# Kernel optimization log

Hardware: AMD Instinct MI355X
Metric: run time of the kernel (lower is better)

Reference implementation:

```python
import jax, jax.numpy as jnp
import numpy as np
import math

B, T, M, C = 4, 2048, 16, 256   # batch, seq, m chunks, c_s chunk width
DIM = 1024                       # layer width; k = DIM // C = 4
D = 64                           # conditioning bottleneck
N_ITERS, TAU = 20, 1.0


def _diag_bias(rows, cols):
    b = np.full((rows, cols), -8.0, dtype=np.float32)
    for i in range(min(rows, cols)):
        b[i, i] = 0.0
    return jnp.asarray(b)


def setup_inputs() -> dict:
    key = jax.random.key(0)
    ks = jax.random.split(key, 10)
    state_dim = M * C
    k = DIM // C
    H_post = np.full((M, k), -8.0, dtype=np.float32)
    for i in range(M):
        H_post[i, i % k] = 0.0
    return {
        "s": jax.random.normal(ks[0], (B, T, M, C), jnp.float32),
        "gamma": 0.02 * jax.random.normal(ks[1], (state_dim,), jnp.float32),
        "compress": 0.02 * jax.random.normal(ks[2], (state_dim, D), jnp.float32),
        "alpha_pre": jnp.float32(0.01),
        "to_logits_pre": 0.02 * jax.random.normal(ks[3], (D, k * M), jnp.float32),
        "H_pre": _diag_bias(k, M),
        "alpha_align": jnp.float32(0.01),
        "to_logits_align": 0.02 * jax.random.normal(ks[4], (D, M * M), jnp.float32),
        "H_align": _diag_bias(M, M),
        "alpha_next": jnp.float32(0.01),
        "to_logits_next": 0.02 * jax.random.normal(ks[5], (D, M * M), jnp.float32),
        "H_next": _diag_bias(M, M),
        "alpha_post": jnp.float32(0.01),
        "to_logits_post": 0.02 * jax.random.normal(ks[6], (D, M * k), jnp.float32),
        "H_post": jnp.asarray(H_post),
        "W_layer": jax.random.normal(ks[7], (DIM, DIM), jnp.float32) / math.sqrt(DIM),
    }


def sinkhorn_log(logits, num_iters=N_ITERS, tau=TAU):
    """Log-domain Sinkhorn; output row-scaled so row sums = 1 * rows-normalized."""
    rows, cols = logits.shape[-2], logits.shape[-1]
    Z = logits / tau
    lr = -math.log(rows)
    lc = -math.log(cols)
    u0 = jnp.zeros(Z.shape[:-1], Z.dtype)
    v0 = jnp.zeros(Z.shape[:-2] + (cols,), Z.dtype)

    def body(_, uv):
        u, v = uv
        u = lr - jax.nn.logsumexp(Z + v[..., None, :], axis=-1)
        v = lc - jax.nn.logsumexp(Z + u[..., None], axis=-2)
        return (u, v)

    u, v = jax.lax.fori_loop(0, num_iters, body, (u0, v0))
    return jnp.exp(Z + u[..., None] + v[..., None, :]) * rows


def _route(code, alpha, to_logits, bias, state, rows, cols):
    """Fused: Sinkhorn(alpha*(code@to_logits)+bias) @ state."""
    raw = (code @ to_logits).reshape(code.shape[:-1] + (rows, cols))
    P = sinkhorn_log(alpha * raw + bias)
    return jnp.einsum('...ij,...jc->...ic', P, state)


def reference(s, gamma, compress, alpha_pre, to_logits_pre, H_pre,
              alpha_align, to_logits_align, H_align,
              alpha_next, to_logits_next, H_next,
              alpha_post, to_logits_post, H_post, W_layer):
    b, t, m, c = s.shape
    state_dim = m * c
    k = W_layer.shape[0] // c
    # RMSNorm over flattened state: F.normalize * sqrt(dim) * (gamma + 1)
    s_vec = s.reshape(b, t, state_dim)
    l2 = jnp.sqrt(jnp.sum(s_vec * s_vec, axis=-1, keepdims=True))
    s_norm = s_vec / jnp.maximum(l2, 1e-12) * jnp.sqrt(jnp.float32(state_dim)) * (gamma + 1.0)
    code = s_norm @ compress  # (b, t, d)
    # read: H_pre (k x m) routes state -> layer input
    layer_in = _route(code, alpha_pre, to_logits_pre, H_pre, s, k, m).reshape(b, t, k * c)
    layer_out = layer_in @ W_layer  # the wrapped layer_fn (dense linear)
    # write: align, absorb output via H_post, prepare next via H_next
    s_aligned = _route(code, alpha_align, to_logits_align, H_align, s, m, m)
    out_flat = layer_out.reshape(b, t, k, c)
    s_updated = s_aligned + _route(code, alpha_post, to_logits_post, H_post, out_flat, m, k)
    s_next = _route(code, alpha_next, to_logits_next, H_next, s_updated, m, m)
    return s_next
```

## Files before the change

kernel.cpp:

```cpp
#include <hip/hip_runtime.h>
#include <math.h>

#define NTOK 8192
#define SD   4096
#define ITERS 20

typedef __attribute__((ext_vector_type(8))) short short8;
typedef __attribute__((ext_vector_type(8))) unsigned short ushort8;
typedef __attribute__((ext_vector_type(4))) unsigned short us4;
typedef __attribute__((ext_vector_type(4))) float f32x4;

__device__ inline unsigned short f2bf(float x) {
    unsigned int u = __float_as_uint(x);
    unsigned int r = (u + 0x7FFFu + ((u >> 16) & 1u)) >> 16;
    return (unsigned short)r;
}
__device__ inline float bf2f(unsigned short u) {
    return __uint_as_float((unsigned int)u << 16);
}
__device__ inline void async_cp16(const void* gsrc, void* ldst) {
    __builtin_amdgcn_global_load_lds(
        (const __attribute__((address_space(1))) unsigned int*)gsrc,
        (__attribute__((address_space(3))) unsigned int*)ldst, 16, 0, 0);
}

__global__ __launch_bounds__(256) void k_preall(const float* __restrict__ W, unsigned short* __restrict__ WT,
                                                const float* __restrict__ compress, const float* __restrict__ gamma,
                                                unsigned short* __restrict__ cgT,
                                                const float* __restrict__ tl_pre, const float* __restrict__ tl_al,
                                                const float* __restrict__ tl_nx,  const float* __restrict__ tl_po,
                                                unsigned short* __restrict__ tlT)
{
    const int b = blockIdx.x;
    const int tid = threadIdx.x;
    if (b < 256) {
        __shared__ float tb[64][65];
        const int k0 = (b >> 4) * 64, n0 = (b & 15) * 64;
        #pragma unroll 4
        for (int q = 0; q < 16; ++q) {
            const int idx = q * 256 + tid;
            const int r = idx >> 6, c = idx & 63;
            tb[r][c] = W[(size_t)(k0 + r) * 1024 + n0 + c];
        }
        __syncthreads();
        #pragma unroll 4
        for (int q = 0; q < 16; ++q) {
            const int idx = q * 256 + tid;
            const int n = idx >> 6, k = idx & 63;
            WT[(size_t)(n0 + n) * 1024 + k0 + k] = f2bf(tb[k][n]);
        }
    } else if (b < 320) {
        __shared__ float tb2[64][65];
        __shared__ float gsh[64];
        const int k0 = (b - 256) * 64;
        #pragma unroll 4
        for (int q = 0; q < 16; ++q) {
            const int idx = q * 256 + tid;
            const int r = idx >> 6, dd = idx & 63;
            tb2[r][dd] = compress[(size_t)(k0 + r) * 64 + dd];
        }
        if (tid < 64) gsh[tid] = gamma[k0 + tid] + 1.0f;
        __syncthreads();
        #pragma unroll 4
        for (int q = 0; q < 16; ++q) {
            const int idx = q * 256 + tid;
            const int d = idx >> 6, r = idx & 63;
            cgT[(size_t)d * SD + k0 + r] = f2bf(tb2[r][d] * gsh[r]);
        }
    } else {
        const int idx = (b - 320) * 256 + tid;
        const int k = idx / 640, n = idx - k * 640;
        float v;
        if (n < 64)       v = tl_pre[k * 64 + n];
        else if (n < 320) v = tl_al[k * 256 + (n - 64)];
        else if (n < 576) v = tl_nx[k * 256 + (n - 320)];
        else              v = tl_po[k * 64 + (n - 576)];
        tlT[(size_t)n * 64 + k] = f2bf(v);
    }
}

__global__ __launch_bounds__(256) void k_code5(const float* __restrict__ s,
                                               const unsigned short* __restrict__ cgT,
                                               float* __restrict__ code_part,
                                               float* __restrict__ ssq_part)
{
    __shared__ float red[4 * 16 * 68];
    __shared__ float ssq_lds[64];
    const int tid  = threadIdx.x;
    const int lane = tid & 63;
    const int wid  = tid >> 6;
    const int q    = blockIdx.x;
    const int tok0 = blockIdx.y * 16;
    const int row  = lane & 15;
    const int kq   = lane >> 4;
    const int wk   = wid * 32;
    const int kbase = q * 1024;

    float ssq = 0.f;
    f32x4 acc[4];
    #pragma unroll
    for (int ni = 0; ni < 4; ++ni) acc[ni] = (f32x4){0.f, 0.f, 0.f, 0.f};

    const float*          srow  = s   + (size_t)(tok0 + row) * SD + kbase + wk + kq * 8;
    const unsigned short* cgrow = cgT + kbase + wk + kq * 8;

    #pragma unroll
    for (int ks = 0; ks < 8; ++ks) {
        const int kg = ks * 128;
        float4 v0 = *(const float4*)(srow + kg);
        float4 v1 = *(const float4*)(srow + kg + 4);
        ssq += v0.x*v0.x + v0.y*v0.y + v0.z*v0.z + v0.w*v0.w
             + v1.x*v1.x + v1.y*v1.y + v1.z*v1.z + v1.w*v1.w;
        short8 a;
        a[0]=(short)f2bf(v0.x); a[1]=(short)f2bf(v0.y); a[2]=(short)f2bf(v0.z); a[3]=(short)f2bf(v0.w);
        a[4]=(short)f2bf(v1.x); a[5]=(short)f2bf(v1.y); a[6]=(short)f2bf(v1.z); a[7]=(short)f2bf(v1.w);
        short8 b[4];
        #pragma unroll
        for (int ni = 0; ni < 4; ++ni)
            b[ni] = *(const short8*)(cgrow + (size_t)(ni * 16 + row) * SD + kg);
        #pragma unroll
        for (int ni = 0; ni < 4; ++ni)
            acc[ni] = __builtin_amdgcn_mfma_f32_16x16x32_bf16(a, b[ni], acc[ni], 0, 0, 0);
    }

    ssq += __shfl_xor(ssq, 16);
    ssq += __shfl_xor(ssq, 32);
    if (lane < 16) ssq_lds[wid * 16 + row] = ssq;

    #pragma unroll
    for (int ni = 0; ni < 4; ++ni)
        #pragma unroll
        for (int r = 0; r < 4; ++r)
            red[wid * 1088 + ((lane >> 4) * 4 + r) * 68 + ni * 16 + (lane & 15)] = acc[ni][r];
    __syncthreads();
    if (tid < 16)
        ssq_part[(size_t)q * NTOK + tok0 + tid] =
            ssq_lds[tid] + ssq_lds[16 + tid] + ssq_lds[32 + tid] + ssq_lds[48 + tid];
    #pragma unroll
    for (int q2 = 0; q2 < 4; ++q2) {
        const int idx = q2 * 256 + tid;
        const int tok = idx >> 6, d = idx & 63;
        float v = red[0 * 1088 + tok * 68 + d] + red[1 * 1088 + tok * 68 + d]
                + red[2 * 1088 + tok * 68 + d] + red[3 * 1088 + tok * 68 + d];
        code_part[((size_t)q * NTOK + tok0 + tok) * 64 + d] = v;
    }
}

#define LGS 660
__global__ __launch_bounds__(256) void k_sink5(const float* __restrict__ s,
                                               const float* __restrict__ code_part,
                                               const float* __restrict__ ssq_part,
                                               const unsigned short* __restrict__ tlT,
                                               const float* __restrict__ a_pre_p, const float* __restrict__ H_pre,
                                               const float* __restrict__ a_al_p,  const float* __restrict__ H_al,
                                               const float* __restrict__ a_nx_p,  const float* __restrict__ H_nx,
                                               const float* __restrict__ a_po_p,  const float* __restrict__ H_po,
                                               unsigned short* __restrict__ layer_in,
                                               float* __restrict__ Pna, float* __restrict__ Pnp)
{
    __shared__ __align__(16) char smem[48576];
    unsigned short* code_sh = (unsigned short*)(smem);
    unsigned short* lg_sh   = (unsigned short*)(smem + 2304);
    float*          Pnx_sh  = (float*)(smem + 2304);
    float*          Pal_sh  = (float*)(smem + 23424);
    float*          Ppo_sh  = (float*)(smem + 40064);
    float*          ssq_sh  = (float*)(smem + 44416);
    float*          Ppre_sh = (float*)(smem + 44480);

    const int tid  = threadIdx.x;
    const int lane = tid & 63;
    const int wid  = tid >> 6;
    const int tok0 = blockIdx.x * 16;

    float cv[4];
    #pragma unroll
    for (int q2 = 0; q2 < 4; ++q2) {
        const int idx = q2 * 256 + tid;
        const size_t off = (size_t)(tok0 + (idx >> 6)) * 64 + (idx & 63);
        cv[q2] = code_part[off] + code_part[(size_t)NTOK * 64 + off]
               + code_part[(size_t)2 * NTOK * 64 + off] + code_part[(size_t)3 * NTOK * 64 + off];
    }
    if (tid < 16) {
        float t = ssq_part[tok0 + tid] + ssq_part[NTOK + tok0 + tid]
                + ssq_part[2 * NTOK + tok0 + tid] + ssq_part[3 * NTOK + tok0 + tid];
        ssq_sh[tid] = 64.0f / fmaxf(sqrtf(t), 1e-12f);
    }
    __syncthreads();
    #pragma unroll
    for (int q2 = 0; q2 < 4; ++q2) {
        const int idx = q2 * 256 + tid;
        code_sh[(idx >> 6) * 72 + (idx & 63)] = f2bf(cv[q2] * ssq_sh[idx >> 6]);
    }
    __syncthreads();

    {
        f32x4 acc2[10];
        #pragma unroll
        for (int ni = 0; ni < 10; ++ni) acc2[ni] = (f32x4){0.f, 0.f, 0.f, 0.f};
        const int nbase = wid * 160;
        #pragma unroll
        for (int ks = 0; ks < 2; ++ks) {
            const int ko = ks * 32 + (lane >> 4) * 8;
            short8 a = *(const short8*)(code_sh + (lane & 15) * 72 + ko);
            #pragma unroll
            for (int ni = 0; ni < 10; ++ni) {
                short8 b = *(const short8*)(tlT + (size_t)(nbase + ni * 16 + (lane & 15)) * 64 + ko);
                acc2[ni] = __builtin_amdgcn_mfma_f32_16x16x32_bf16(a, b, acc2[ni], 0, 0, 0);
            }
        }
        #pragma unroll
        for (int ni = 0; ni < 10; ++ni)
            #pragma unroll
            for (int r = 0; r < 4; ++r)
                lg_sh[((lane >> 4) * 4 + r) * LGS + nbase + ni * 16 + (lane & 15)] = f2bf(acc2[ni][r]);
    }
    __syncthreads();

    const int t_in = lane >> 2;
    const int sub  = lane & 3;
    float Km[4][16];

    if (wid < 2) {
        const unsigned short* lgp = lg_sh + t_in * LGS + (wid == 0 ? 64 : 320) + sub * 64;
        #pragma unroll
        for (int rr = 0; rr < 4; ++rr)
            #pragma unroll
            for (int h = 0; h < 2; ++h) {
                ushort8 rv = *(const ushort8*)(lgp + rr * 16 + h * 8);
                #pragma unroll
                for (int e = 0; e < 8; ++e) Km[rr][h * 8 + e] = bf2f(rv[e]);
            }
    } else if (wid == 2) {
        const unsigned short* lgp = lg_sh + t_in * LGS + sub * 16;
        #pragma unroll
        for (int h = 0; h < 2; ++h) {
            ushort8 rv = *(const ushort8*)(lgp + h * 8);
            #pragma unroll
            for (int e = 0; e < 8; ++e) Km[0][h * 8 + e] = bf2f(rv[e]);
        }
    } else {
        const unsigned short* lgp = lg_sh + t_in * LGS + 576 + sub * 16;
        #pragma unroll
        for (int rr = 0; rr < 4; ++rr) {
            us4 rv = *(const us4*)(lgp + rr * 4);
            #pragma unroll
            for (int e = 0; e < 4; ++e) Km[rr][e] = bf2f(rv[e]);
        }
    }
    __syncthreads();

    if (wid < 2) {
        const float alpha = (wid == 0) ? (*a_al_p) : (*a_nx_p);
        const float* Hp   = ((wid == 0) ? H_al : H_nx) + sub * 64;
        #pragma unroll
        for (int rr = 0; rr < 4; ++rr)
            #pragma unroll
            for (int c = 0; c < 16; ++c)
                Km[rr][c] = __expf(alpha * Km[rr][c] + Hp[rr * 16 + c]);
        float v[16], u[4];
        #pragma unroll
        for (int c = 0; c < 16; ++c) v[c] = 1.0f;
        for (int it = 0; it < ITERS; ++it) {
            #pragma unroll
            for (int rr = 0; rr < 4; ++rr) {
                float su = 0.f;
                #pragma unroll
                for (int c = 0; c < 16; ++c) su += Km[rr][c] * v[c];
                u[rr] = 0.0625f * __builtin_amdgcn_rcpf(su);
            }
            float pv[16];
            #pragma unroll
            for (int c = 0; c < 16; ++c)
                pv[c] = Km[0][c]*u[0] + Km[1][c]*u[1] + Km[2][c]*u[2] + Km[3][c]*u[3];
            #pragma unroll
            for (int c = 0; c < 16; ++c) pv[c] += __shfl_xor(pv[c], 1);
            #pragma unroll
            for (int c = 0; c < 16; ++c) pv[c] += __shfl_xor(pv[c], 2);
            #pragma unroll
            for (int c = 0; c < 16; ++c) v[c] = 0.0625f * __builtin_amdgcn_rcpf(pv[c]);
        }
        float* dst = ((wid == 0) ? Pal_sh : Pnx_sh) + t_in * 260;
        #pragma unroll
        for (int rr = 0; rr < 4; ++rr) {
            const float su16 = 16.0f * u[rr];
            #pragma unroll
            for (int c = 0; c < 16; ++c)
                dst[(sub * 4 + rr) * 16 + c] = Km[rr][c] * su16 * v[c];
        }
    } else if (wid == 2) {
        const float alpha = *a_pre_p;
        const float* Hp  = H_pre + sub * 16;
        #pragma unroll
        for (int c = 0; c < 16; ++c) Km[0][c] = __expf(alpha * Km[0][c] + Hp[c]);
        float v[16], u;
        #pragma unroll
        for (int c = 0; c < 16; ++c) v[c] = 1.0f;
        for (int it = 0; it < ITERS; ++it) {
            float su = 0.f;
            #pragma unroll
            for (int c = 0; c < 16; ++c) su += Km[0][c] * v[c];
            u = 0.25f * __builtin_amdgcn_rcpf(su);
            float pv[16];
            #pragma unroll
            for (int c = 0; c < 16; ++c) pv[c] = Km[0][c] * u;
            #pragma unroll
            for (int c = 0; c < 16; ++c) pv[c] += __shfl_xor(pv[c], 1);
            #pragma unroll
            for (int c = 0; c < 16; ++c) pv[c] += __shfl_xor(pv[c], 2);
            #pragma unroll
            for (int c = 0; c < 16; ++c) v[c] = 0.0625f * __builtin_amdgcn_rcpf(pv[c]);
        }
        const float su4 = 4.0f * u;
        #pragma unroll
        for (int c = 0; c < 16; ++c)
            Ppre_sh[t_in * 64 + sub * 16 + c] = Km[0][c] * su4 * v[c];
    } else {
        const float alpha = *a_po_p;
        const float* Hp  = H_po + sub * 16;
        #pragma unroll
        for (int rr = 0; rr < 4; ++rr)
            #pragma unroll
            for (int c = 0; c < 4; ++c)
                Km[rr][c] = __expf(alpha * Km[rr][c] + Hp[rr * 4 + c]);
        float v[4], u[4];
        #pragma unroll
        for (int c = 0; c < 4; ++c) v[c] = 1.0f;
        for (int it = 0; it < ITERS; ++it) {
            #pragma unroll
            for (int rr = 0; rr < 4; ++rr) {
                float su = 0.f;
                #pragma unroll
                for (int c = 0; c < 4; ++c) su += Km[rr][c] * v[c];
                u[rr] = 0.0625f * __builtin_amdgcn_rcpf(su);
            }
            float pv[4];
            #pragma unroll
            for (int c = 0; c < 4; ++c)
                pv[c] = Km[0][c]*u[0] + Km[1][c]*u[1] + Km[2][c]*u[2] + Km[3][c]*u[3];
            #pragma unroll
            for (int c = 0; c < 4; ++c) pv[c] += __shfl_xor(pv[c], 1);
            #pragma unroll
            for (int c = 0; c < 4; ++c) pv[c] += __shfl_xor(pv[c], 2);
            #pragma unroll
            for (int c = 0; c < 4; ++c) v[c] = 0.25f * __builtin_amdgcn_rcpf(pv[c]);
        }
        #pragma unroll
        for (int rr = 0; rr < 4; ++rr) {
            const float su16 = 16.0f * u[rr];
            #pragma unroll
            for (int c = 0; c < 4; ++c)
                Ppo_sh[t_in * 68 + (sub * 4 + rr) * 4 + c] = Km[rr][c] * su16 * v[c];
        }
    }
    __syncthreads();

    const int ct = tid >> 4;
    const int cj = tid & 15;
    {
        const float* pnx = Pnx_sh + ct * 260;
        const float* pal = Pal_sh + ct * 260;
        const float* ppo = Ppo_sh + ct * 68;
        #pragma unroll
        for (int m = 0; m < 16; ++m) {
            float a2 = 0.f;
            #pragma unroll
            for (int t2 = 0; t2 < 16; ++t2) a2 += pnx[m * 16 + t2] * pal[t2 * 16 + cj];
            Pna[(size_t)(tok0 + ct) * 256 + m * 16 + cj] = a2;
        }
        #pragma unroll
        for (int e = 0; e < 4; ++e) {
            const int idx = cj * 4 + e;
            const int m = idx >> 2, q = idx & 3;
            float a2 = 0.f;
            #pragma unroll
            for (int t2 = 0; t2 < 16; ++t2) a2 += pnx[m * 16 + t2] * ppo[t2 * 4 + q];
            Pnp[(size_t)(tok0 + ct) * 64 + idx] = a2;
        }
    }

    #pragma unroll
    for (int g = 0; g < 4; ++g) {
        const int t = g * 4 + wid;
        const float4* sp = (const float4*)(s + (size_t)(tok0 + t) * SD) + lane;
        const float* pp = Ppre_sh + t * 64;
        f32x4 acc4[4];
        #pragma unroll
        for (int i = 0; i < 4; ++i) acc4[i] = (f32x4){0.f, 0.f, 0.f, 0.f};
        #pragma unroll
        for (int jh = 0; jh < 2; ++jh) {
            float4 sv[8];
            #pragma unroll
            for (int j = 0; j < 8; ++j) sv[j] = sp[(jh * 8 + j) * 64];
            #pragma unroll
            for (int i = 0; i < 4; ++i)
                #pragma unroll
                for (int j = 0; j < 8; ++j) {
                    const float pij = pp[i * 16 + jh * 8 + j];
                    acc4[i][0] += pij * sv[j].x;
                    acc4[i][1] += pij * sv[j].y;
                    acc4[i][2] += pij * sv[j].z;
                    acc4[i][3] += pij * sv[j].w;
                }
        }
        unsigned short* lo = layer_in + (size_t)(tok0 + t) * 1024 + lane * 4;
        #pragma unroll
        for (int i = 0; i < 4; ++i) {
            us4 o;
            o[0] = f2bf(acc4[i][0]); o[1] = f2bf(acc4[i][1]);
            o[2] = f2bf(acc4[i][2]); o[3] = f2bf(acc4[i][3]);
            *(us4*)(lo + i * 256) = o;
        }
    }
}

__global__ __launch_bounds__(256) void k_gemm_bf16(const unsigned short* __restrict__ A,
                                                   const unsigned short* __restrict__ BT,
                                                   unsigned short* __restrict__ Cb)
{
    __shared__ unsigned short Abuf[128 * 48];
    __shared__ unsigned short Bbuf[128 * 48];
    const int tid  = threadIdx.x;
    const int lane = tid & 63;
    const int wid  = tid >> 6;
    const int wr   = wid >> 1, wc = wid & 1;
    const int m0 = blockIdx.y * 128, n0 = blockIdx.x * 128;

    f32x4 acc[4][4];
    #pragma unroll
    for (int mi = 0; mi < 4; ++mi)
        #pragma unroll
        for (int ni = 0; ni < 4; ++ni) acc[mi][ni] = (f32x4){0.f, 0.f, 0.f, 0.f};

    for (int k0 = 0; k0 < 1024; k0 += 32) {
        __syncthreads();
        #pragma unroll
        for (int h = 0; h < 2; ++h) {
            const int idx = h * 256 + tid;
            const int row = idx >> 2, kq = idx & 3;
            float4 av = *(const float4*)(A + (size_t)(m0 + row) * 1024 + k0 + kq * 8);
            *(float4*)(Abuf + row * 48 + kq * 8) = av;
            float4 bv = *(const float4*)(BT + (size_t)(n0 + row) * 1024 + k0 + kq * 8);
            *(float4*)(Bbuf + row * 48 + kq * 8) = bv;
        }
        __syncthreads();

        short8 a[4], b[4];
        #pragma unroll
        for (int mi = 0; mi < 4; ++mi)
            a[mi] = *(const short8*)(Abuf + (wr * 64 + mi * 16 + (lane & 15)) * 48 + (lane >> 4) * 8);
        #pragma unroll
        for (int ni = 0; ni < 4; ++ni)
            b[ni] = *(const short8*)(Bbuf + (wc * 64 + ni * 16 + (lane & 15)) * 48 + (lane >> 4) * 8);
        #pragma unroll
        for (int mi = 0; mi < 4; ++mi)
            #pragma unroll
            for (int ni = 0; ni < 4; ++ni)
                acc[mi][ni] = __builtin_amdgcn_mfma_f32_16x16x32_bf16(a[mi], b[ni], acc[mi][ni], 0, 0, 0);
    }

    #pragma unroll
    for (int mi = 0; mi < 4; ++mi)
        #pragma unroll
        for (int ni = 0; ni < 4; ++ni)
            #pragma unroll
            for (int r = 0; r < 4; ++r)
                Cb[(size_t)(m0 + wr * 64 + mi * 16 + (lane >> 4) * 4 + r) * 1024 +
                   n0 + wc * 64 + ni * 16 + (lane & 15)] = f2bf(acc[mi][ni][r]);
}

__global__ __launch_bounds__(256) void k_final3(const float* __restrict__ s,
                                                const unsigned short* __restrict__ lo_bf,
                                                const float* __restrict__ Pna,
                                                const float* __restrict__ Pnp,
                                                float* __restrict__ out)
{
    __shared__ __align__(16) float s_sh[SD];
    __shared__ __align__(16) unsigned short lo_sh[1024];
    __shared__ float Pna_sh[256];
    __shared__ float Pnp_sh[64];
    const int tid  = threadIdx.x;
    const int lane = tid & 63;
    const int wid  = tid >> 6;
    const int tok  = blockIdx.x;

    const float* gbase = s + (size_t)tok * SD + wid * 1024 + lane * 4;
    #pragma unroll
    for (int c = 0; c < 4; ++c)
        async_cp16(gbase + c * 256, s_sh + wid * 1024 + c * 256);
    if (wid < 2)
        async_cp16(lo_bf + (size_t)tok * 1024 + wid * 512 + lane * 8, lo_sh + wid * 512);
    Pna_sh[tid] = Pna[(size_t)tok * 256 + tid];
    if (tid < 64) Pnp_sh[tid] = Pnp[(size_t)tok * 64 + tid];
    __syncthreads();

    const int c = tid;
    float lov[4];
    #pragma unroll
    for (int q = 0; q < 4; ++q) lov[q] = bf2f(lo_sh[q * 256 + c]);
    #pragma unroll
    for (int m = 0; m < 16; ++m) {
        float acc = 0.f;
        #pragma unroll
        for (int j = 0; j < 16; ++j) acc += Pna_sh[m * 16 + j] * s_sh[j * 256 + c];
        #pragma unroll
        for (int q = 0; q < 4; ++q) acc += Pnp_sh[m * 4 + q] * lov[q];
        out[(size_t)tok * SD + m * 256 + c] = acc;
    }
}

extern "C" void kernel_launch(void* const* d_in, const int* in_sizes, int n_in,
                              void* d_out, int out_size, void* d_ws, size_t ws_size,
                              hipStream_t stream)
{
    const float* s        = (const float*)d_in[0];
    const float* gamma    = (const float*)d_in[1];
    const float* compress = (const float*)d_in[2];
    const float* a_pre    = (const float*)d_in[3];
    const float* tl_pre   = (const float*)d_in[4];
    const float* H_pre    = (const float*)d_in[5];
    const float* a_al     = (const float*)d_in[6];
    const float* tl_al    = (const float*)d_in[7];
    const float* H_al     = (const float*)d_in[8];
    const float* a_nx     = (const float*)d_in[9];
    const float* tl_nx    = (const float*)d_in[10];
    const float* H_nx     = (const float*)d_in[11];
    const float* a_po     = (const float*)d_in[12];
    const float* tl_po    = (const float*)d_in[13];
    const float* H_po     = (const float*)d_in[14];
    const float* W        = (const float*)d_in[15];
    float* out = (float*)d_out;

    char* p = (char*)d_ws;
    unsigned short* lo_bf    = (unsigned short*)p; p += (size_t)8192 * 1024 * 2;
    float* Pna               = (float*)p;          p += (size_t)8192 * 256 * 4;
    float* Pnp               = (float*)p;          p += (size_t)8192 * 64 * 4;
    unsigned short* layer_in = (unsigned short*)p; p += (size_t)8192 * 1024 * 2;
    unsigned short* WT       = (unsigned short*)p; p += (size_t)1024 * 1024 * 2;
    unsigned short* cgT      = (unsigned short*)p; p += (size_t)64 * SD * 2;
    unsigned short* tlT      = (unsigned short*)p; p += (size_t)640 * 64 * 2 + 128;
    float* code_part         = (float*)p;          p += (size_t)4 * NTOK * 64 * 4;
    float* ssq_part          = (float*)p;          p += (size_t)4 * NTOK * 4;

    k_preall<<<480, 256, 0, stream>>>(W, WT, compress, gamma, cgT,
                                      tl_pre, tl_al, tl_nx, tl_po, tlT);
    k_code5<<<dim3(4, 512), 256, 0, stream>>>(s, cgT, code_part, ssq_part);
    k_sink5<<<512, 256, 0, stream>>>(s, code_part, ssq_part, tlT,
                                     a_pre, H_pre, a_al, H_al,
                                     a_nx, H_nx, a_po, H_po,
                                     layer_in, Pna, Pnp);
    k_gemm_bf16<<<dim3(8, 64), 256, 0, stream>>>(layer_in, WT, lo_bf);
    k_final3<<<NTOK, 256, 0, stream>>>(s, lo_bf, Pna, Pnp, out);
}
```

Measured before the change: 185.6 us.

## Cache a bf16 copy of the state for the routing and final kernels

```diff
diff --git a/kernel.cpp b/kernel.cpp
--- a/kernel.cpp
+++ b/kernel.cpp
@@ -79,10 +79,11 @@
     }
 }
 
-__global__ __launch_bounds__(256) void k_code5(const float* __restrict__ s,
+__global__ __launch_bounds__(256) void k_code6(const float* __restrict__ s,
                                                const unsigned short* __restrict__ cgT,
                                                float* __restrict__ code_part,
-                                               float* __restrict__ ssq_part)
+                                               float* __restrict__ ssq_part,
+                                               unsigned short* __restrict__ s_bf)
 {
     __shared__ float red[4 * 16 * 68];
     __shared__ float ssq_lds[64];
@@ -101,7 +102,8 @@
     #pragma unroll
     for (int ni = 0; ni < 4; ++ni) acc[ni] = (f32x4){0.f, 0.f, 0.f, 0.f};
 
-    const float*          srow  = s   + (size_t)(tok0 + row) * SD + kbase + wk + kq * 8;
+    const float*          srow  = s    + (size_t)(tok0 + row) * SD + kbase + wk + kq * 8;
+    unsigned short*       sbrow = s_bf + (size_t)(tok0 + row) * SD + kbase + wk + kq * 8;
     const unsigned short* cgrow = cgT + kbase + wk + kq * 8;
 
     #pragma unroll
@@ -114,6 +116,7 @@
         short8 a;
         a[0]=(short)f2bf(v0.x); a[1]=(short)f2bf(v0.y); a[2]=(short)f2bf(v0.z); a[3]=(short)f2bf(v0.w);
         a[4]=(short)f2bf(v1.x); a[5]=(short)f2bf(v1.y); a[6]=(short)f2bf(v1.z); a[7]=(short)f2bf(v1.w);
+        if (s_bf) *(short8*)(sbrow + kg) = a;
         short8 b[4];
         #pragma unroll
         for (int ni = 0; ni < 4; ++ni)
@@ -147,7 +150,9 @@
 }
 
 #define LGS 660
-__global__ __launch_bounds__(256) void k_sink5(const float* __restrict__ s,
+template<bool SBF>
+__global__ __launch_bounds__(256) void k_sink6(const float* __restrict__ s,
+                                               const unsigned short* __restrict__ s_bf,
                                                const float* __restrict__ code_part,
                                                const float* __restrict__ ssq_part,
                                                const unsigned short* __restrict__ tlT,
@@ -378,37 +383,80 @@
         }
     }
 
-    #pragma unroll
-    for (int g = 0; g < 4; ++g) {
-        const int t = g * 4 + wid;
-        const float4* sp = (const float4*)(s + (size_t)(tok0 + t) * SD) + lane;
-        const float* pp = Ppre_sh + t * 64;
-        f32x4 acc4[4];
-        #pragma unroll
-        for (int i = 0; i < 4; ++i) acc4[i] = (f32x4){0.f, 0.f, 0.f, 0.f};
-        #pragma unroll
-        for (int jh = 0; jh < 2; ++jh) {
-            float4 sv[8];
-            #pragma unroll
-            for (int j = 0; j < 8; ++j) sv[j] = sp[(jh * 8 + j) * 64];
+    if (SBF) {
+        const int half = lane >> 5;
+        const int c8   = lane & 31;
+        #pragma unroll
+        for (int g = 0; g < 2; ++g) {
+            const int t = g * 8 + wid * 2 + half;
+            const ushort8* tb = (const ushort8*)(s_bf + (size_t)(tok0 + t) * SD);
+            const float* pp = Ppre_sh + t * 64;
+            float accv[4][8];
             #pragma unroll
             for (int i = 0; i < 4; ++i)
                 #pragma unroll
-                for (int j = 0; j < 8; ++j) {
-                    const float pij = pp[i * 16 + jh * 8 + j];
-                    acc4[i][0] += pij * sv[j].x;
-                    acc4[i][1] += pij * sv[j].y;
-                    acc4[i][2] += pij * sv[j].z;
-                    acc4[i][3] += pij * sv[j].w;
-                }
-        }
-        unsigned short* lo = layer_in + (size_t)(tok0 + t) * 1024 + lane * 4;
-        #pragma unroll
-        for (int i = 0; i < 4; ++i) {
-            us4 o;
-            o[0] = f2bf(acc4[i][0]); o[1] = f2bf(acc4[i][1]);
-            o[2] = f2bf(acc4[i][2]); o[3] = f2bf(acc4[i][3]);
-            *(us4*)(lo + i * 256) = o;
+                for (int e = 0; e < 8; ++e) accv[i][e] = 0.f;
+            #pragma unroll
+            for (int jh = 0; jh < 2; ++jh) {
+                ushort8 sv[8];
+                #pragma unroll
+                for (int j = 0; j < 8; ++j) sv[j] = tb[(jh * 8 + j) * 32 + c8];
+                float sf[8][8];
+                #pragma unroll
+                for (int j = 0; j < 8; ++j)
+                    #pragma unroll
+                    for (int e = 0; e < 8; ++e) sf[j][e] = bf2f(sv[j][e]);
+                #pragma unroll
+                for (int i = 0; i < 4; ++i)
+                    #pragma unroll
+                    for (int j = 0; j < 8; ++j) {
+                        const float pij = pp[i * 16 + jh * 8 + j];
+                        #pragma unroll
+                        for (int e = 0; e < 8; ++e) accv[i][e] += pij * sf[j][e];
+                    }
+            }
+            unsigned short* lo = layer_in + (size_t)(tok0 + t) * 1024 + c8 * 8;
+            #pragma unroll
+            for (int i = 0; i < 4; ++i) {
+                ushort8 o;
+                #pragma unroll
+                for (int e = 0; e < 8; ++e) o[e] = f2bf(accv[i][e]);
+                *(ushort8*)(lo + i * 256) = o;
+            }
+        }
+    } else {
+        #pragma unroll
+        for (int g = 0; g < 4; ++g) {
+            const int t = g * 4 + wid;
+            const float4* sp = (const float4*)(s + (size_t)(tok0 + t) * SD) + lane;
+            const float* pp = Ppre_sh + t * 64;
+            f32x4 acc4[4];
+            #pragma unroll
+            for (int i = 0; i < 4; ++i) acc4[i] = (f32x4){0.f, 0.f, 0.f, 0.f};
+            #pragma unroll
+            for (int jh = 0; jh < 2; ++jh) {
+                float4 sv[8];
+                #pragma unroll
+                for (int j = 0; j < 8; ++j) sv[j] = sp[(jh * 8 + j) * 64];
+                #pragma unroll
+                for (int i = 0; i < 4; ++i)
+                    #pragma unroll
+                    for (int j = 0; j < 8; ++j) {
+                        const float pij = pp[i * 16 + jh * 8 + j];
+                        acc4[i][0] += pij * sv[j].x;
+                        acc4[i][1] += pij * sv[j].y;
+                        acc4[i][2] += pij * sv[j].z;
+                        acc4[i][3] += pij * sv[j].w;
+                    }
+            }
+            unsigned short* lo = layer_in + (size_t)(tok0 + t) * 1024 + lane * 4;
+            #pragma unroll
+            for (int i = 0; i < 4; ++i) {
+                us4 o;
+                o[0] = f2bf(acc4[i][0]); o[1] = f2bf(acc4[i][1]);
+                o[2] = f2bf(acc4[i][2]); o[3] = f2bf(acc4[i][3]);
+                *(us4*)(lo + i * 256) = o;
+            }
         }
     }
 }
@@ -468,7 +516,9 @@
                    n0 + wc * 64 + ni * 16 + (lane & 15)] = f2bf(acc[mi][ni][r]);
 }
 
-__global__ __launch_bounds__(256) void k_final3(const float* __restrict__ s,
+template<bool SBF>
+__global__ __launch_bounds__(256) void k_final4(const float* __restrict__ s,
+                                                const unsigned short* __restrict__ s_bf,
                                                 const unsigned short* __restrict__ lo_bf,
                                                 const float* __restrict__ Pna,
                                                 const float* __restrict__ Pnp,
@@ -483,10 +533,22 @@
     const int wid  = tid >> 6;
     const int tok  = blockIdx.x;
 
-    const float* gbase = s + (size_t)tok * SD + wid * 1024 + lane * 4;
-    #pragma unroll
-    for (int c = 0; c < 4; ++c)
-        async_cp16(gbase + c * 256, s_sh + wid * 1024 + c * 256);
+    if (SBF) {
+        #pragma unroll
+        for (int c2 = 0; c2 < 2; ++c2) {
+            ushort8 v = *(const ushort8*)(s_bf + (size_t)tok * SD + c2 * 2048 + tid * 8);
+            float4 f0, f1;
+            f0.x = bf2f(v[0]); f0.y = bf2f(v[1]); f0.z = bf2f(v[2]); f0.w = bf2f(v[3]);
+            f1.x = bf2f(v[4]); f1.y = bf2f(v[5]); f1.z = bf2f(v[6]); f1.w = bf2f(v[7]);
+            *(float4*)(s_sh + c2 * 2048 + tid * 8)     = f0;
+            *(float4*)(s_sh + c2 * 2048 + tid * 8 + 4) = f1;
+        }
+    } else {
+        const float* gbase = s + (size_t)tok * SD + wid * 1024 + lane * 4;
+        #pragma unroll
+        for (int c = 0; c < 4; ++c)
+            async_cp16(gbase + c * 256, s_sh + wid * 1024 + c * 256);
+    }
     if (wid < 2)
         async_cp16(lo_bf + (size_t)tok * 1024 + wid * 512 + lane * 8, lo_sh + wid * 512);
     Pna_sh[tid] = Pna[(size_t)tok * 256 + tid];
@@ -531,23 +593,39 @@
     float* out = (float*)d_out;
 
     char* p = (char*)d_ws;
-    unsigned short* lo_bf    = (unsigned short*)p; p += (size_t)8192 * 1024 * 2;
-    float* Pna               = (float*)p;          p += (size_t)8192 * 256 * 4;
-    float* Pnp               = (float*)p;          p += (size_t)8192 * 64 * 4;
+    unsigned short* s_bf     = (unsigned short*)p; p += (size_t)NTOK * SD * 2;
     unsigned short* layer_in = (unsigned short*)p; p += (size_t)8192 * 1024 * 2;
     unsigned short* WT       = (unsigned short*)p; p += (size_t)1024 * 1024 * 2;
     unsigned short* cgT      = (unsigned short*)p; p += (size_t)64 * SD * 2;
     unsigned short* tlT      = (unsigned short*)p; p += (size_t)640 * 64 * 2 + 128;
-    float* code_part         = (float*)p;          p += (size_t)4 * NTOK * 64 * 4;
-    float* ssq_part          = (float*)p;          p += (size_t)4 * NTOK * 4;
+    float* Pna               = (float*)p;          p += (size_t)8192 * 256 * 4;
+    float* Pnp               = (float*)p;          p += (size_t)8192 * 64 * 4;
+    char* uregion            = p;
+    float* code_part         = (float*)uregion;
+    float* ssq_part          = (float*)(uregion + (size_t)4 * NTOK * 64 * 4);
+    unsigned short* lo_bf    = (unsigned short*)uregion;
+    p = uregion + (size_t)8192 * 1024 * 2;
+    const bool use_sbf = ((size_t)(p - (char*)d_ws) <= ws_size);
 
     k_preall<<<480, 256, 0, stream>>>(W, WT, compress, gamma, cgT,
                                       tl_pre, tl_al, tl_nx, tl_po, tlT);
-    k_code5<<<dim3(4, 512), 256, 0, stream>>>(s, cgT, code_part, ssq_part);
-    k_sink5<<<512, 256, 0, stream>>>(s, code_part, ssq_part, tlT,
-                                     a_pre, H_pre, a_al, H_al,
-                                     a_nx, H_nx, a_po, H_po,
-                                     layer_in, Pna, Pnp);
+    k_code6<<<dim3(4, 512), 256, 0, stream>>>(s, cgT, code_part, ssq_part,
+                                              use_sbf ? s_bf : (unsigned short*)nullptr);
+    if (use_sbf) {
+        k_sink6<true><<<512, 256, 0, stream>>>(s, s_bf, code_part, ssq_part, tlT,
+                                               a_pre, H_pre, a_al, H_al,
+                                               a_nx, H_nx, a_po, H_po,
+                                               layer_in, Pna, Pnp);
+    } else {
+        k_sink6<false><<<512, 256, 0, stream>>>(s, s_bf, code_part, ssq_part, tlT,
+                                                a_pre, H_pre, a_al, H_al,
+                                                a_nx, H_nx, a_po, H_po,
+                                                layer_in, Pna, Pnp);
+    }
     k_gemm_bf16<<<dim3(8, 64), 256, 0, stream>>>(layer_in, WT, lo_bf);
-    k_final3<<<NTOK, 256, 0, stream>>>(s, lo_bf, Pna, Pnp, out);
-}
+    if (use_sbf) {
+        k_final4<true><<<NTOK, 256, 0, stream>>>(s, s_bf, lo_bf, Pna, Pnp, out);
+    } else {
+        k_final4<false><<<NTOK, 256, 0, stream>>>(s, s_bf, lo_bf, Pna, Pnp, out);
+    }
+}
```

After: 207.8 us. 1.12x slower.
